# Optimization experiments

Hardware: AMD Instinct MI355X
Metric: run time of the kernel (lower is better)

The kernel has to match this reference:

```python
import jax, jax.numpy as jnp
import numpy as np

N = 50000
E = 800000
IN_DIM = 16
OUT_DIM = 16
EDGE_IN = 16
HID = 32


def setup_inputs() -> dict:
    key = jax.random.key(0)
    ks = jax.random.split(key, 9)
    x = jax.random.normal(ks[0], (N, IN_DIM), dtype=jnp.float32)
    edge_index = jax.random.randint(ks[1], (2, E), 0, N, dtype=jnp.int64)
    edge_attr = jax.random.normal(ks[2], (E, EDGE_IN), dtype=jnp.float32)
    # edge MLP params: Linear(EDGE_IN, 32) -> ReLU -> Linear(32, IN*OUT)
    w1 = jax.random.normal(ks[3], (EDGE_IN, HID), dtype=jnp.float32) * (1.0 / np.sqrt(EDGE_IN))
    b1 = jnp.zeros((HID,), dtype=jnp.float32)
    w2 = jax.random.normal(ks[4], (HID, IN_DIM * OUT_DIM), dtype=jnp.float32) * (1.0 / np.sqrt(HID))
    b2 = jnp.zeros((IN_DIM * OUT_DIM,), dtype=jnp.float32)
    # NNConv root weight and bias (defaults root_weight=True, bias=True)
    root = jax.random.normal(ks[5], (IN_DIM, OUT_DIM), dtype=jnp.float32) * (1.0 / np.sqrt(IN_DIM))
    bias = jnp.zeros((OUT_DIM,), dtype=jnp.float32)
    return {"x": x, "edge_index": edge_index, "edge_attr": edge_attr,
            "w1": w1, "b1": b1, "w2": w2, "b2": b2, "root": root, "bias": bias}


def reference(x, edge_index, edge_attr, w1, b1, w2, b2, root, bias):
    src = edge_index[0]  # x_j gathered from source nodes
    dst = edge_index[1]  # scatter-mean into target nodes
    # edge MLP -> per-edge weight matrix [E, IN, OUT]
    h = jax.nn.relu(edge_attr @ w1 + b1)
    W = (h @ w2 + b2).reshape(-1, IN_DIM, OUT_DIM)
    # per-edge matvec: message_e = x[src_e] @ W_e  -> [E, OUT]
    msg = jnp.einsum('ei,eio->eo', x[src], W)
    # scatter-mean aggregate into N target nodes
    summed = jax.ops.segment_sum(msg, dst, num_segments=N)
    cnt = jax.ops.segment_sum(jnp.ones((msg.shape[0],), dtype=msg.dtype), dst, num_segments=N)
    aggr = summed / jnp.maximum(cnt, 1.0)[:, None]
    return aggr + x @ root + bias
```

## Files before the change

kernel.cpp:

```cpp
#include <hip/hip_runtime.h>
#include <hip/hip_bf16.h>
#include <hip/hip_fp16.h>


#define N_NODES 50000
#define N_EDGES 800000
#define IN_D    16
#define OUT_D   16
#define HID_D   32
#define NBLK_E  (N_EDGES / 256)
#define NBLK_G  (N_NODES * OUT_D / 256)
#define KTILES  17

typedef __attribute__((ext_vector_type(8))) _Float16 hfrag8;
typedef __attribute__((ext_vector_type(4))) float f32x4;

__device__ __forceinline__ void fma4(float a, const float4 w, float4& m) {
    m.x = fmaf(a, w.x, m.x);
    m.y = fmaf(a, w.y, m.y);
    m.z = fmaf(a, w.z, m.z);
    m.w = fmaf(a, w.w, m.w);
}
__device__ __forceinline__ int clampn(int v) {
    return v < 0 ? 0 : (v >= N_NODES ? N_NODES - 1 : v);
}


template <int MODE, int CAP>
__global__ __launch_bounds__(256) void edge_k(
    const float* __restrict__ x,
    const int*   __restrict__ ei,
    const float* __restrict__ ea,
    const float* __restrict__ w1,
    const float* __restrict__ b1,
    const float* __restrict__ w2,
    const float* __restrict__ b2,
    int*   __restrict__ aux,
    int*   __restrict__ next,
    float* __restrict__ msg)
{
    __shared__ hfrag8 s_B[KTILES * 64];
    __shared__ __half s_h[4 * HID_D * 64];
    __shared__ float4 s_w1[IN_D * HID_D / 4];
    __shared__ float4 s_b1[HID_D / 4];

    const int t    = threadIdx.x;
    const int lane = t & 63;
    const int w    = t >> 6;
    const int e    = blockIdx.x * 256 + t;

    {
        const float4* w1v = reinterpret_cast<const float4*>(w1);
        const float4* b1v = reinterpret_cast<const float4*>(b1);
        if (t < IN_D * HID_D / 4) s_w1[t] = w1v[t];
        if (t < HID_D / 4)        s_b1[t] = b1v[t];

        __half* bp = reinterpret_cast<__half*>(s_B);
        for (int r = t; r < KTILES * 32; r += 256) {
            const int tile = r >> 5, q = (r >> 3) & 3, j = r & 7;
            const int base = ((tile * 4 + q) * 16) * 8 + j;
            float vals[16];
            if (r < 512) {
                const float4* wr = reinterpret_cast<const float4*>(w2) + r * 4;
                float4 v0 = wr[0], v1 = wr[1], v2 = wr[2], v3 = wr[3];
                vals[0]=v0.x; vals[1]=v0.y; vals[2]=v0.z; vals[3]=v0.w;
                vals[4]=v1.x; vals[5]=v1.y; vals[6]=v1.z; vals[7]=v1.w;
                vals[8]=v2.x; vals[9]=v2.y; vals[10]=v2.z; vals[11]=v2.w;
                vals[12]=v3.x; vals[13]=v3.y; vals[14]=v3.z; vals[15]=v3.w;
            } else if (r < 528) {
                const float4* br = reinterpret_cast<const float4*>(b2) + (r - 512) * 4;
                float4 v0 = br[0], v1 = br[1], v2 = br[2], v3 = br[3];
                vals[0]=v0.x; vals[1]=v0.y; vals[2]=v0.z; vals[3]=v0.w;
                vals[4]=v1.x; vals[5]=v1.y; vals[6]=v1.z; vals[7]=v1.w;
                vals[8]=v2.x; vals[9]=v2.y; vals[10]=v2.z; vals[11]=v2.w;
                vals[12]=v3.x; vals[13]=v3.y; vals[14]=v3.z; vals[15]=v3.w;
            } else {
                #pragma unroll
                for (int o = 0; o < 16; ++o) vals[o] = 0.f;
            }
            #pragma unroll
            for (int o = 0; o < 16; ++o) bp[base + o * 8] = __float2half(vals[o]);
        }
    }

    const int src = clampn(ei[e]);
    const int dst = clampn(ei[N_EDGES + e]);
    int slot;
    if (MODE == 0) {
        int rank = atomicAdd(&aux[dst], 1);
        rank = rank < CAP ? rank : CAP - 1;
        slot = dst * CAP + rank;
    } else {
        next[e] = atomicExch(&aux[dst * 4 + (e & 3)], e);
        slot = e;
    }

    const int q   = lane >> 4;
    const int n   = lane & 15;
    const int qh  = q >> 1;
    const int i0q = (q & 1) * 8;
    float4 xpre[4][2];
    #pragma unroll
    for (int sub = 0; sub < 4; ++sub) {
        const int srcB = __shfl(src, sub * 16 + n, 64);
        const float4* xp = reinterpret_cast<const float4*>(x) + (size_t)srcB * 4 + (i0q >> 2);
        xpre[sub][0] = xp[0];
        xpre[sub][1] = xp[1];
    }

    __syncthreads();

    {
        float eav[IN_D];
        {
            const float4* eap = reinterpret_cast<const float4*>(ea) + (size_t)e * 4;
            float4 a0 = eap[0], a1 = eap[1], a2 = eap[2], a3 = eap[3];
            eav[0]=a0.x;  eav[1]=a0.y;  eav[2]=a0.z;  eav[3]=a0.w;
            eav[4]=a1.x;  eav[5]=a1.y;  eav[6]=a1.z;  eav[7]=a1.w;
            eav[8]=a2.x;  eav[9]=a2.y;  eav[10]=a2.z; eav[11]=a2.w;
            eav[12]=a3.x; eav[13]=a3.y; eav[14]=a3.z; eav[15]=a3.w;
        }
        float4 hv[HID_D / 4];
        #pragma unroll
        for (int j = 0; j < HID_D / 4; ++j) hv[j] = s_b1[j];
        #pragma unroll
        for (int i = 0; i < IN_D; ++i) {
            const float xi = eav[i];
            #pragma unroll
            for (int j = 0; j < HID_D / 4; ++j) fma4(xi, s_w1[i * (HID_D / 4) + j], hv[j]);
        }
        __half* hw = &s_h[w * (HID_D * 64)];
        #pragma unroll
        for (int j = 0; j < HID_D / 4; ++j) {
            hw[(4*j+0)*64 + lane] = __float2half(fmaxf(hv[j].x, 0.f));
            hw[(4*j+1)*64 + lane] = __float2half(fmaxf(hv[j].y, 0.f));
            hw[(4*j+2)*64 + lane] = __float2half(fmaxf(hv[j].z, 0.f));
            hw[(4*j+3)*64 + lane] = __float2half(fmaxf(hv[j].w, 0.f));
        }
    }
    asm volatile("s_waitcnt lgkmcnt(0)" ::: "memory");
    __builtin_amdgcn_wave_barrier();

    const __half* hw = &s_h[w * (HID_D * 64)];
    #pragma unroll
    for (int sub = 0; sub < 4; ++sub) {
        const int posW = sub * 16 + n;
        __half2 xh[4];
        {
            float4 xa = xpre[sub][0], xb = xpre[sub][1];
            xh[0] = __float22half2_rn(make_float2(xa.x, xa.y));
            xh[1] = __float22half2_rn(make_float2(xa.z, xa.w));
            xh[2] = __float22half2_rn(make_float2(xb.x, xb.y));
            xh[3] = __float22half2_rn(make_float2(xb.z, xb.w));
        }
        f32x4 acc = {0.f, 0.f, 0.f, 0.f};
        #pragma unroll
        for (int tile = 0; tile < 16; ++tile) {
            const int k = 2 * tile + qh;
            const __half2 hh = __half2half2(hw[k * 64 + posW]);
            union { hfrag8 v; __half2 h[4]; } a;
            a.h[0] = __hmul2(hh, xh[0]);
            a.h[1] = __hmul2(hh, xh[1]);
            a.h[2] = __hmul2(hh, xh[2]);
            a.h[3] = __hmul2(hh, xh[3]);
            acc = __builtin_amdgcn_mfma_f32_16x16x32_f16(a.v, s_B[tile * 64 + lane], acc, 0, 0, 0);
        }
        {
            union { hfrag8 v; __half2 h[4]; } a;
            if (qh == 0) { a.h[0]=xh[0]; a.h[1]=xh[1]; a.h[2]=xh[2]; a.h[3]=xh[3]; }
            else { hfrag8 z = {0,0,0,0,0,0,0,0}; a.v = z; }
            acc = __builtin_amdgcn_mfma_f32_16x16x32_f16(a.v, s_B[16 * 64 + lane], acc, 0, 0, 0);
        }
        #pragma unroll
        for (int r = 0; r < 4; ++r) {
            const int slotB = __shfl(slot, sub * 16 + q * 4 + r, 64);
            msg[(size_t)slotB * 16 + n] = acc[r];
        }
    }
}


template <int CAP>
__global__ __launch_bounds__(256) void gather_cap(
    const float* __restrict__ x,
    const float* __restrict__ root,
    const float* __restrict__ bias,
    const float* __restrict__ msg,
    const int*   __restrict__ cnt,
    float* __restrict__ out)
{
    __shared__ float s_root[IN_D * OUT_D];
    __shared__ float s_bias[OUT_D];
    const int t = threadIdx.x;
    s_root[t] = root[t];
    if (t < OUT_D) s_bias[t] = bias[t];
    __syncthreads();

    const int g = blockIdx.x * 256 + t;
    const int n = g >> 4;
    const int o = g & 15;

    const int d = cnt[n];
    const int m = d < CAP ? d : CAP;
    const float* base = msg + (size_t)n * CAP * 16 + o;

    float a0 = 0.f, a1 = 0.f, a2 = 0.f, a3 = 0.f;
    int j = 0;
    for (; j + 4 <= m; j += 4) {
        a0 += base[(j + 0) * 16];
        a1 += base[(j + 1) * 16];
        a2 += base[(j + 2) * 16];
        a3 += base[(j + 3) * 16];
    }
    for (; j < m; ++j) a0 += base[j * 16];
    const float acc = (a0 + a1) + (a2 + a3);

    const float inv = 1.0f / (float)(d > 1 ? d : 1);
    float mv = acc * inv + s_bias[o];

    float xs[IN_D];
    {
        const float4* xp = reinterpret_cast<const float4*>(x) + (size_t)n * 4;
        float4 b0 = xp[0], b1v = xp[1], b2v = xp[2], b3 = xp[3];
        xs[0]=b0.x;  xs[1]=b0.y;  xs[2]=b0.z;  xs[3]=b0.w;
        xs[4]=b1v.x; xs[5]=b1v.y; xs[6]=b1v.z; xs[7]=b1v.w;
        xs[8]=b2v.x; xs[9]=b2v.y; xs[10]=b2v.z; xs[11]=b2v.w;
        xs[12]=b3.x; xs[13]=b3.y; xs[14]=b3.z; xs[15]=b3.w;
    }
    #pragma unroll
    for (int i = 0; i < IN_D; ++i)
        mv = fmaf(xs[i], s_root[i * OUT_D + o], mv);

    out[(size_t)n * OUT_D + o] = mv;
}


__global__ __launch_bounds__(256) void gather_ll4(
    const float* __restrict__ x,
    const float* __restrict__ root,
    const float* __restrict__ bias,
    const float* __restrict__ msg,
    const int*   __restrict__ head4,
    const int*   __restrict__ next,
    float* __restrict__ out)
{
    __shared__ float4 s_root4[IN_D * 4];
    __shared__ float4 s_bias4[4];
    const int t = threadIdx.x;
    if (t < IN_D * 4) s_root4[t] = reinterpret_cast<const float4*>(root)[t];
    if (t < 4)        s_bias4[t] = reinterpret_cast<const float4*>(bias)[t];
    __syncthreads();

    const int g = blockIdx.x * 256 + t;
    const int n = g >> 4;
    const int l = t & 15;
    const int c = l >> 2;
    const int p = l & 3;

    float4 acc = make_float4(0.f, 0.f, 0.f, 0.f);
    int cnt = 0;
    int j = head4[n * 4 + c];
    while (j >= 0) {
        const float4 v = reinterpret_cast<const float4*>(msg + (size_t)j * 16)[p];
        acc.x += v.x; acc.y += v.y; acc.z += v.z; acc.w += v.w;
        ++cnt;
        j = next[j];
    }

    acc.x += __shfl_xor(acc.x, 4); acc.y += __shfl_xor(acc.y, 4);
    acc.z += __shfl_xor(acc.z, 4); acc.w += __shfl_xor(acc.w, 4);
    cnt   += __shfl_xor(cnt, 4);
    acc.x += __shfl_xor(acc.x, 8); acc.y += __shfl_xor(acc.y, 8);
    acc.z += __shfl_xor(acc.z, 8); acc.w += __shfl_xor(acc.w, 8);
    cnt   += __shfl_xor(cnt, 8);

    const float inv = 1.0f / (float)(cnt > 1 ? cnt : 1);
    float4 m = s_bias4[p];
    m.x += acc.x * inv; m.y += acc.y * inv; m.z += acc.z * inv; m.w += acc.w * inv;

    {
        const float4* xp = reinterpret_cast<const float4*>(x) + (size_t)n * 4;
        float4 x0 = xp[0], x1 = xp[1], x2 = xp[2], x3 = xp[3];
        const float xs[IN_D] = { x0.x,x0.y,x0.z,x0.w, x1.x,x1.y,x1.z,x1.w,
                                 x2.x,x2.y,x2.z,x2.w, x3.x,x3.y,x3.z,x3.w };
        #pragma unroll
        for (int i = 0; i < IN_D; ++i) fma4(xs[i], s_root4[i * 4 + p], m);
    }

    if (c == 0)
        reinterpret_cast<float4*>(out + (size_t)n * 16)[p] = m;
}

extern "C" void kernel_launch(void* const* d_in, const int* in_sizes, int n_in,
                              void* d_out, int out_size, void* d_ws, size_t ws_size,
                              hipStream_t stream) {
    const float* x    = (const float*)d_in[0];
    const int*   ei   = (const int*)  d_in[1];
    const float* ea   = (const float*)d_in[2];
    const float* w1   = (const float*)d_in[3];
    const float* b1   = (const float*)d_in[4];
    const float* w2   = (const float*)d_in[5];
    const float* b2   = (const float*)d_in[6];
    const float* root = (const float*)d_in[7];
    const float* bias = (const float*)d_in[8];
    float* out = (float*)d_out;

    const size_t need64 = (size_t)N_NODES * 4 + (size_t)N_NODES * 64 * 64;
    const size_t need48 = (size_t)N_NODES * 4 + (size_t)N_NODES * 48 * 64;

    if (ws_size >= need64) {
        int*   cnt = (int*)d_ws;
        float* msg = (float*)(cnt + N_NODES);
        hipMemsetAsync(cnt, 0, N_NODES * sizeof(int), stream);
        edge_k<0, 64> <<<NBLK_E, 256, 0, stream>>>(x, ei, ea, w1, b1, w2, b2, cnt, nullptr, msg);
        gather_cap<64><<<NBLK_G, 256, 0, stream>>>(x, root, bias, msg, cnt, out);
    } else if (ws_size >= need48) {
        int*   cnt = (int*)d_ws;
        float* msg = (float*)(cnt + N_NODES);
        hipMemsetAsync(cnt, 0, N_NODES * sizeof(int), stream);
        edge_k<0, 48> <<<NBLK_E, 256, 0, stream>>>(x, ei, ea, w1, b1, w2, b2, cnt, nullptr, msg);
        gather_cap<48><<<NBLK_G, 256, 0, stream>>>(x, root, bias, msg, cnt, out);
    } else {
        int*   head4 = (int*)d_ws;
        int*   next  = head4 + N_NODES * 4;
        float* msg   = (float*)(next + N_EDGES);
        edge_k<1, 0> <<<NBLK_E, 256, 0, stream>>>(x, ei, ea, w1, b1, w2, b2, head4, next, msg);
        gather_ll4   <<<NBLK_G, 256, 0, stream>>>(x, root, bias, msg, head4, next, out);
    }
}
```

Baseline: 186.1 us.

## Precompute weight blob once, async-load to LDS, larger edge blocks, vectorized gather

Adds a one-block setup kernel that converts w2/b2 into the fp16 MFMA fragment layout and packs it with w1/b1 into a workspace blob. Each edge block then copies the blob into LDS with global_load_lds instead of redoing the fp32-to-fp16 conversion per block. Edge blocks grow to 512 threads. The hidden activations are stored per edge row with an XOR swizzle, so each lane reads its 16 hidden values as two vector loads instead of 16 scalar LDS reads. The gather kernel now reads float4 message rows across four lanes and reduces with shuffles. The cost is an extra kernel launch and 20KB of LDS per block.

```diff
diff --git a/kernel.cpp b/kernel.cpp
--- a/kernel.cpp
+++ b/kernel.cpp
@@ -8,9 +8,13 @@
 #define IN_D    16
 #define OUT_D   16
 #define HID_D   32
-#define NBLK_E  (N_EDGES / 256)
+#define KTILES  17
 #define NBLK_G  (N_NODES * OUT_D / 256)
-#define KTILES  17
+#define EDGE_TPB   512
+#define NBLK_E512  ((N_EDGES + EDGE_TPB - 1) / EDGE_TPB)
+#define BLOB_BYTES 20480
+#define BLOB_W1    17408
+#define BLOB_B1    19456
 
 typedef __attribute__((ext_vector_type(8))) _Float16 hfrag8;
 typedef __attribute__((ext_vector_type(4))) float f32x4;
@@ -24,102 +28,124 @@
 __device__ __forceinline__ int clampn(int v) {
     return v < 0 ? 0 : (v >= N_NODES ? N_NODES - 1 : v);
 }
-
-
-template <int MODE, int CAP>
-__global__ __launch_bounds__(256) void edge_k(
-    const float* __restrict__ x,
-    const int*   __restrict__ ei,
-    const float* __restrict__ ea,
+__device__ __forceinline__ void gload_lds16(const void* g, void* l) {
+    __builtin_amdgcn_global_load_lds(
+        (const __attribute__((address_space(1))) unsigned int*)g,
+        (__attribute__((address_space(3))) unsigned int*)l,
+        16, 0, 0);
+}
+
+
+__global__ __launch_bounds__(256) void setup_k(
     const float* __restrict__ w1,
     const float* __restrict__ b1,
     const float* __restrict__ w2,
     const float* __restrict__ b2,
+    unsigned char* __restrict__ blob)
+{
+    const int t = threadIdx.x;
+    __half* bp = reinterpret_cast<__half*>(blob);
+    for (int r = t; r < KTILES * 32; r += 256) {
+        const int tile = r >> 5, q = (r >> 3) & 3, j = r & 7;
+        const int base = ((tile * 4 + q) * 16) * 8 + j;
+        float vals[16];
+        if (r < 512) {
+            const float4* wr = reinterpret_cast<const float4*>(w2) + r * 4;
+            float4 v0 = wr[0], v1 = wr[1], v2 = wr[2], v3 = wr[3];
+            vals[0]=v0.x; vals[1]=v0.y; vals[2]=v0.z; vals[3]=v0.w;
+            vals[4]=v1.x; vals[5]=v1.y; vals[6]=v1.z; vals[7]=v1.w;
+            vals[8]=v2.x; vals[9]=v2.y; vals[10]=v2.z; vals[11]=v2.w;
+            vals[12]=v3.x; vals[13]=v3.y; vals[14]=v3.z; vals[15]=v3.w;
+        } else if (r < 528) {
+            const float4* br = reinterpret_cast<const float4*>(b2) + (r - 512) * 4;
+            float4 v0 = br[0], v1 = br[1], v2 = br[2], v3 = br[3];
+            vals[0]=v0.x; vals[1]=v0.y; vals[2]=v0.z; vals[3]=v0.w;
+            vals[4]=v1.x; vals[5]=v1.y; vals[6]=v1.z; vals[7]=v1.w;
+            vals[8]=v2.x; vals[9]=v2.y; vals[10]=v2.z; vals[11]=v2.w;
+            vals[12]=v3.x; vals[13]=v3.y; vals[14]=v3.z; vals[15]=v3.w;
+        } else {
+            #pragma unroll
+            for (int o = 0; o < 16; ++o) vals[o] = 0.f;
+        }
+        #pragma unroll
+        for (int o = 0; o < 16; ++o) bp[base + o * 8] = __float2half(vals[o]);
+    }
+    float* wf = reinterpret_cast<float*>(blob + BLOB_W1);
+    wf[t] = w1[t];
+    wf[t + 256] = w1[t + 256];
+    if (t < HID_D) reinterpret_cast<float*>(blob + BLOB_B1)[t] = b1[t];
+}
+
+
+template <int MODE, int CAP>
+__global__ __launch_bounds__(EDGE_TPB, 6) void edge_k(
+    const float* __restrict__ x,
+    const int*   __restrict__ ei,
+    const float* __restrict__ ea,
+    const unsigned char* __restrict__ gblob,
     int*   __restrict__ aux,
     int*   __restrict__ next,
     float* __restrict__ msg)
 {
-    __shared__ hfrag8 s_B[KTILES * 64];
-    __shared__ __half s_h[4 * HID_D * 64];
-    __shared__ float4 s_w1[IN_D * HID_D / 4];
-    __shared__ float4 s_b1[HID_D / 4];
+    __shared__ alignas(16) unsigned char s_blob[BLOB_BYTES];
+    __shared__ alignas(16) __half s_h2[8 * 64 * 32];
 
     const int t    = threadIdx.x;
     const int lane = t & 63;
     const int w    = t >> 6;
-    const int e    = blockIdx.x * 256 + t;
-
-    {
-        const float4* w1v = reinterpret_cast<const float4*>(w1);
-        const float4* b1v = reinterpret_cast<const float4*>(b1);
-        if (t < IN_D * HID_D / 4) s_w1[t] = w1v[t];
-        if (t < HID_D / 4)        s_b1[t] = b1v[t];
-
-        __half* bp = reinterpret_cast<__half*>(s_B);
-        for (int r = t; r < KTILES * 32; r += 256) {
-            const int tile = r >> 5, q = (r >> 3) & 3, j = r & 7;
-            const int base = ((tile * 4 + q) * 16) * 8 + j;
-            float vals[16];
-            if (r < 512) {
-                const float4* wr = reinterpret_cast<const float4*>(w2) + r * 4;
-                float4 v0 = wr[0], v1 = wr[1], v2 = wr[2], v3 = wr[3];
-                vals[0]=v0.x; vals[1]=v0.y; vals[2]=v0.z; vals[3]=v0.w;
-                vals[4]=v1.x; vals[5]=v1.y; vals[6]=v1.z; vals[7]=v1.w;
-                vals[8]=v2.x; vals[9]=v2.y; vals[10]=v2.z; vals[11]=v2.w;
-                vals[12]=v3.x; vals[13]=v3.y; vals[14]=v3.z; vals[15]=v3.w;
-            } else if (r < 528) {
-                const float4* br = reinterpret_cast<const float4*>(b2) + (r - 512) * 4;
-                float4 v0 = br[0], v1 = br[1], v2 = br[2], v3 = br[3];
-                vals[0]=v0.x; vals[1]=v0.y; vals[2]=v0.z; vals[3]=v0.w;
-                vals[4]=v1.x; vals[5]=v1.y; vals[6]=v1.z; vals[7]=v1.w;
-                vals[8]=v2.x; vals[9]=v2.y; vals[10]=v2.z; vals[11]=v2.w;
-                vals[12]=v3.x; vals[13]=v3.y; vals[14]=v3.z; vals[15]=v3.w;
-            } else {
-                #pragma unroll
-                for (int o = 0; o < 16; ++o) vals[o] = 0.f;
-            }
-            #pragma unroll
-            for (int o = 0; o < 16; ++o) bp[base + o * 8] = __float2half(vals[o]);
-        }
-    }
-
-    const int src = clampn(ei[e]);
-    const int dst = clampn(ei[N_EDGES + e]);
-    int slot;
-    if (MODE == 0) {
-        int rank = atomicAdd(&aux[dst], 1);
-        rank = rank < CAP ? rank : CAP - 1;
-        slot = dst * CAP + rank;
-    } else {
-        next[e] = atomicExch(&aux[dst * 4 + (e & 3)], e);
-        slot = e;
-    }
+    const int e    = blockIdx.x * EDGE_TPB + t;
+    const bool wvalid = (blockIdx.x * EDGE_TPB + w * 64) < N_EDGES;
+
+    #pragma unroll
+    for (int j = 0; j < 3; ++j) {
+        const int ch = w + 8 * j;
+        if (ch < BLOB_BYTES / 1024)
+            gload_lds16(gblob + ch * 1024 + lane * 16, s_blob + ch * 1024);
+    }
+
+    const hfrag8* s_B  = reinterpret_cast<const hfrag8*>(s_blob);
+    const float4* s_w1 = reinterpret_cast<const float4*>(s_blob + BLOB_W1);
+    const float4* s_b1 = reinterpret_cast<const float4*>(s_blob + BLOB_B1);
 
     const int q   = lane >> 4;
     const int n   = lane & 15;
     const int qh  = q >> 1;
     const int i0q = (q & 1) * 8;
+
+    int slot = 0;
     float4 xpre[4][2];
-    #pragma unroll
-    for (int sub = 0; sub < 4; ++sub) {
-        const int srcB = __shfl(src, sub * 16 + n, 64);
-        const float4* xp = reinterpret_cast<const float4*>(x) + (size_t)srcB * 4 + (i0q >> 2);
-        xpre[sub][0] = xp[0];
-        xpre[sub][1] = xp[1];
+    float eav[IN_D];
+
+    if (wvalid) {
+        const int src = clampn(ei[e]);
+        const int dst = clampn(ei[N_EDGES + e]);
+        if (MODE == 0) {
+            int rank = atomicAdd(&aux[dst], 1);
+            rank = rank < CAP ? rank : CAP - 1;
+            slot = dst * CAP + rank;
+        } else {
+            next[e] = atomicExch(&aux[dst * 4 + (e & 3)], e);
+            slot = e;
+        }
+        #pragma unroll
+        for (int sub = 0; sub < 4; ++sub) {
+            const int srcB = __shfl(src, sub * 16 + n, 64);
+            const float4* xp = reinterpret_cast<const float4*>(x) + (size_t)srcB * 4 + (i0q >> 2);
+            xpre[sub][0] = xp[0];
+            xpre[sub][1] = xp[1];
+        }
+        const float4* eap = reinterpret_cast<const float4*>(ea) + (size_t)e * 4;
+        float4 a0 = eap[0], a1 = eap[1], a2 = eap[2], a3 = eap[3];
+        eav[0]=a0.x;  eav[1]=a0.y;  eav[2]=a0.z;  eav[3]=a0.w;
+        eav[4]=a1.x;  eav[5]=a1.y;  eav[6]=a1.z;  eav[7]=a1.w;
+        eav[8]=a2.x;  eav[9]=a2.y;  eav[10]=a2.z; eav[11]=a2.w;
+        eav[12]=a3.x; eav[13]=a3.y; eav[14]=a3.z; eav[15]=a3.w;
     }
 
     __syncthreads();
+    if (!wvalid) return;
 
     {
-        float eav[IN_D];
-        {
-            const float4* eap = reinterpret_cast<const float4*>(ea) + (size_t)e * 4;
-            float4 a0 = eap[0], a1 = eap[1], a2 = eap[2], a3 = eap[3];
-            eav[0]=a0.x;  eav[1]=a0.y;  eav[2]=a0.z;  eav[3]=a0.w;
-            eav[4]=a1.x;  eav[5]=a1.y;  eav[6]=a1.z;  eav[7]=a1.w;
-            eav[8]=a2.x;  eav[9]=a2.y;  eav[10]=a2.z; eav[11]=a2.w;
-            eav[12]=a3.x; eav[13]=a3.y; eav[14]=a3.z; eav[15]=a3.w;
-        }
         float4 hv[HID_D / 4];
         #pragma unroll
         for (int j = 0; j < HID_D / 4; ++j) hv[j] = s_b1[j];
@@ -129,19 +155,26 @@
             #pragma unroll
             for (int j = 0; j < HID_D / 4; ++j) fma4(xi, s_w1[i * (HID_D / 4) + j], hv[j]);
         }
-        __half* hw = &s_h[w * (HID_D * 64)];
-        #pragma unroll
-        for (int j = 0; j < HID_D / 4; ++j) {
-            hw[(4*j+0)*64 + lane] = __float2half(fmaxf(hv[j].x, 0.f));
-            hw[(4*j+1)*64 + lane] = __float2half(fmaxf(hv[j].y, 0.f));
-            hw[(4*j+2)*64 + lane] = __float2half(fmaxf(hv[j].z, 0.f));
-            hw[(4*j+3)*64 + lane] = __float2half(fmaxf(hv[j].w, 0.f));
-        }
+        union { hfrag8 v[4]; __half h[32]; } hp;
+        #pragma unroll
+        for (int jj = 0; jj < 8; ++jj) {
+            const int k0 = 4 * jj;
+            hp.h[((k0 + 0) & 1) * 16 + ((k0 + 0) >> 1)] = __float2half(fmaxf(hv[jj].x, 0.f));
+            hp.h[((k0 + 1) & 1) * 16 + ((k0 + 1) >> 1)] = __float2half(fmaxf(hv[jj].y, 0.f));
+            hp.h[((k0 + 2) & 1) * 16 + ((k0 + 2) >> 1)] = __float2half(fmaxf(hv[jj].z, 0.f));
+            hp.h[((k0 + 3) & 1) * 16 + ((k0 + 3) >> 1)] = __float2half(fmaxf(hv[jj].w, 0.f));
+        }
+        hfrag8* rowv = reinterpret_cast<hfrag8*>(s_h2 + (size_t)w * 2048 + lane * 32);
+        const int swl = (lane >> 1) & 3;
+        rowv[0 ^ swl] = hp.v[0];
+        rowv[1 ^ swl] = hp.v[1];
+        rowv[2 ^ swl] = hp.v[2];
+        rowv[3 ^ swl] = hp.v[3];
     }
     asm volatile("s_waitcnt lgkmcnt(0)" ::: "memory");
     __builtin_amdgcn_wave_barrier();
 
-    const __half* hw = &s_h[w * (HID_D * 64)];
+    const __half* hbase = s_h2 + (size_t)w * 2048;
     #pragma unroll
     for (int sub = 0; sub < 4; ++sub) {
         const int posW = sub * 16 + n;
@@ -153,11 +186,18 @@
             xh[2] = __float22half2_rn(make_float2(xb.x, xb.y));
             xh[3] = __float22half2_rn(make_float2(xb.z, xb.w));
         }
+        union { hfrag8 v; __half h[8]; } hA, hB;
+        {
+            const hfrag8* rowv = reinterpret_cast<const hfrag8*>(hbase + posW * 32);
+            const int swr = (posW >> 1) & 3;
+            hA.v = rowv[(2 * qh + 0) ^ swr];
+            hB.v = rowv[(2 * qh + 1) ^ swr];
+        }
         f32x4 acc = {0.f, 0.f, 0.f, 0.f};
         #pragma unroll
         for (int tile = 0; tile < 16; ++tile) {
-            const int k = 2 * tile + qh;
-            const __half2 hh = __half2half2(hw[k * 64 + posW]);
+            const __half hs = (tile < 8) ? hA.h[tile] : hB.h[tile - 8];
+            const __half2 hh = __half2half2(hs);
             union { hfrag8 v; __half2 h[4]; } a;
             a.h[0] = __hmul2(hh, xh[0]);
             a.h[1] = __hmul2(hh, xh[1]);
@@ -189,49 +229,58 @@
     const int*   __restrict__ cnt,
     float* __restrict__ out)
 {
-    __shared__ float s_root[IN_D * OUT_D];
-    __shared__ float s_bias[OUT_D];
+    __shared__ float4 s_root4[IN_D * 4];
+    __shared__ float4 s_bias4[4];
     const int t = threadIdx.x;
-    s_root[t] = root[t];
-    if (t < OUT_D) s_bias[t] = bias[t];
+    if (t < IN_D * 4) s_root4[t] = reinterpret_cast<const float4*>(root)[t];
+    if (t < 4)        s_bias4[t] = reinterpret_cast<const float4*>(bias)[t];
     __syncthreads();
 
     const int g = blockIdx.x * 256 + t;
     const int n = g >> 4;
-    const int o = g & 15;
+    const int l = t & 15;
+    const int c = l >> 2;
+    const int p = l & 3;
 
     const int d = cnt[n];
     const int m = d < CAP ? d : CAP;
-    const float* base = msg + (size_t)n * CAP * 16 + o;
-
-    float a0 = 0.f, a1 = 0.f, a2 = 0.f, a3 = 0.f;
-    int j = 0;
-    for (; j + 4 <= m; j += 4) {
-        a0 += base[(j + 0) * 16];
-        a1 += base[(j + 1) * 16];
-        a2 += base[(j + 2) * 16];
-        a3 += base[(j + 3) * 16];
-    }
-    for (; j < m; ++j) a0 += base[j * 16];
-    const float acc = (a0 + a1) + (a2 + a3);
+
+    const float4* base = reinterpret_cast<const float4*>(msg) + (size_t)n * CAP * 4 + p;
+    float4 a0 = make_float4(0.f, 0.f, 0.f, 0.f);
+    float4 a1 = make_float4(0.f, 0.f, 0.f, 0.f);
+    int j = c;
+    for (; j + 4 < m; j += 8) {
+        float4 v0 = base[(size_t)j * 4];
+        float4 v1 = base[(size_t)(j + 4) * 4];
+        a0.x += v0.x; a0.y += v0.y; a0.z += v0.z; a0.w += v0.w;
+        a1.x += v1.x; a1.y += v1.y; a1.z += v1.z; a1.w += v1.w;
+    }
+    if (j < m) {
+        float4 v0 = base[(size_t)j * 4];
+        a0.x += v0.x; a0.y += v0.y; a0.z += v0.z; a0.w += v0.w;
+    }
+    float4 acc = make_float4(a0.x + a1.x, a0.y + a1.y, a0.z + a1.z, a0.w + a1.w);
+
+    acc.x += __shfl_xor(acc.x, 4); acc.y += __shfl_xor(acc.y, 4);
+    acc.z += __shfl_xor(acc.z, 4); acc.w += __shfl_xor(acc.w, 4);
+    acc.x += __shfl_xor(acc.x, 8); acc.y += __shfl_xor(acc.y, 8);
+    acc.z += __shfl_xor(acc.z, 8); acc.w += __shfl_xor(acc.w, 8);
 
     const float inv = 1.0f / (float)(d > 1 ? d : 1);
-    float mv = acc * inv + s_bias[o];
-
-    float xs[IN_D];
+    float4 mv = s_bias4[p];
+    mv.x += acc.x * inv; mv.y += acc.y * inv; mv.z += acc.z * inv; mv.w += acc.w * inv;
+
     {
         const float4* xp = reinterpret_cast<const float4*>(x) + (size_t)n * 4;
-        float4 b0 = xp[0], b1v = xp[1], b2v = xp[2], b3 = xp[3];
-        xs[0]=b0.x;  xs[1]=b0.y;  xs[2]=b0.z;  xs[3]=b0.w;
-        xs[4]=b1v.x; xs[5]=b1v.y; xs[6]=b1v.z; xs[7]=b1v.w;
-        xs[8]=b2v.x; xs[9]=b2v.y; xs[10]=b2v.z; xs[11]=b2v.w;
-        xs[12]=b3.x; xs[13]=b3.y; xs[14]=b3.z; xs[15]=b3.w;
-    }
-    #pragma unroll
-    for (int i = 0; i < IN_D; ++i)
-        mv = fmaf(xs[i], s_root[i * OUT_D + o], mv);
-
-    out[(size_t)n * OUT_D + o] = mv;
+        float4 x0 = xp[0], x1 = xp[1], x2 = xp[2], x3 = xp[3];
+        const float xs[IN_D] = { x0.x,x0.y,x0.z,x0.w, x1.x,x1.y,x1.z,x1.w,
+                                 x2.x,x2.y,x2.z,x2.w, x3.x,x3.y,x3.z,x3.w };
+        #pragma unroll
+        for (int i = 0; i < IN_D; ++i) fma4(xs[i], s_root4[i * 4 + p], mv);
+    }
+
+    if (c == 0)
+        reinterpret_cast<float4*>(out + (size_t)n * 16)[p] = mv;
 }
 
 
@@ -305,26 +354,30 @@
     const float* bias = (const float*)d_in[8];
     float* out = (float*)d_out;
 
-    const size_t need64 = (size_t)N_NODES * 4 + (size_t)N_NODES * 64 * 64;
-    const size_t need48 = (size_t)N_NODES * 4 + (size_t)N_NODES * 48 * 64;
+    unsigned char* blob = (unsigned char*)d_ws;
+
+    const size_t need64 = (size_t)BLOB_BYTES + (size_t)N_NODES * 4 + (size_t)N_NODES * 64 * 64;
+    const size_t need48 = (size_t)BLOB_BYTES + (size_t)N_NODES * 4 + (size_t)N_NODES * 48 * 64;
+
+    setup_k<<<1, 256, 0, stream>>>(w1, b1, w2, b2, blob);
 
     if (ws_size >= need64) {
-        int*   cnt = (int*)d_ws;
-        float* msg = (float*)(cnt + N_NODES);
+        int*   cnt = (int*)(blob + BLOB_BYTES);
+        float* msg = (float*)(blob + BLOB_BYTES + (size_t)N_NODES * 4);
         hipMemsetAsync(cnt, 0, N_NODES * sizeof(int), stream);
-        edge_k<0, 64> <<<NBLK_E, 256, 0, stream>>>(x, ei, ea, w1, b1, w2, b2, cnt, nullptr, msg);
+        edge_k<0, 64><<<NBLK_E512, EDGE_TPB, 0, stream>>>(x, ei, ea, blob, cnt, nullptr, msg);
         gather_cap<64><<<NBLK_G, 256, 0, stream>>>(x, root, bias, msg, cnt, out);
     } else if (ws_size >= need48) {
-        int*   cnt = (int*)d_ws;
-        float* msg = (float*)(cnt + N_NODES);
+        int*   cnt = (int*)(blob + BLOB_BYTES);
+        float* msg = (float*)(blob + BLOB_BYTES + (size_t)N_NODES * 4);
         hipMemsetAsync(cnt, 0, N_NODES * sizeof(int), stream);
-        edge_k<0, 48> <<<NBLK_E, 256, 0, stream>>>(x, ei, ea, w1, b1, w2, b2, cnt, nullptr, msg);
+        edge_k<0, 48><<<NBLK_E512, EDGE_TPB, 0, stream>>>(x, ei, ea, blob, cnt, nullptr, msg);
         gather_cap<48><<<NBLK_G, 256, 0, stream>>>(x, root, bias, msg, cnt, out);
     } else {
-        int*   head4 = (int*)d_ws;
+        int*   head4 = (int*)(blob + BLOB_BYTES);
         int*   next  = head4 + N_NODES * 4;
         float* msg   = (float*)(next + N_EDGES);
-        edge_k<1, 0> <<<NBLK_E, 256, 0, stream>>>(x, ei, ea, w1, b1, w2, b2, head4, next, msg);
-        gather_ll4   <<<NBLK_G, 256, 0, stream>>>(x, root, bias, msg, head4, next, out);
-    }
-}
+        edge_k<1, 0><<<NBLK_E512, EDGE_TPB, 0, stream>>>(x, ei, ea, blob, head4, next, msg);
+        gather_ll4  <<<NBLK_G, 256, 0, stream>>>(x, root, bias, msg, head4, next, out);
+    }
+}
```

Result: slower. 195.2 us (+4.9%).
